# Performance work log

Measured on AMD Instinct MI355X. Metric: run time of the kernel, lower is better.

## Reference

```python
import jax, jax.numpy as jnp
import numpy as np

B, S, D = 32, 200, 256          # batch, seq_len (hard-coded 200), emb_dim (hard-coded 256)
H_CLS, H_TNS, H = 2, 4, 6       # classical heads, tensor heads, total (rate=1/3, num_heads=6)
DFF, VOCAB, L, TD = 1024, 3500, 8, 2


def layer_norm(x, g, b, eps=1e-6):
    m = x.mean(-1, keepdims=True)
    v = ((x - m) ** 2).mean(-1, keepdims=True)
    return (x - m) * jax.lax.rsqrt(v + eps) * g + b


def setup_inputs() -> dict:
    key = jax.random.key(0)
    ks = jax.random.split(key, 12)
    n = jax.random.normal
    s1 = 1.0 / np.sqrt(4 + TD - 1.0)       # TNLayer RandomNormal stddev for A1/A4
    s2 = 1.0 / np.sqrt(4 + 2 * TD - 1.0)   # for A2/A3
    return {
        "tokens": jax.random.randint(ks[0], (B, S), 0, VOCAB),
        "tok_emb": n(ks[1], (VOCAB, D)) * 0.02,
        "pos_emb": n(ks[2], (S, D)) * 0.02,
        # stacked over L layers; axis 1 of size 3 is (q, k, v)
        "wqkv_w": n(ks[3], (L, 3, D, 2 * D)) * 0.05,
        "wqkv_b": jnp.zeros((L, 3, 2 * D)),
        "A1": n(ks[4], (L, 3, 4, TD, 4)) * s1,
        "A2": n(ks[5], (L, 3, 4, TD, TD, 8)) * s2,
        "A3": n(ks[6], (L, 3, 4, TD, TD, 8)) * s2,
        "A4": n(ks[7], (L, 3, 4, TD, 4)) * s1,
        "tnb": jnp.zeros((L, 3, 4 * D)),
        "out_w": n(ks[8], (L, H * D, D)) * 0.02,
        "out_b": jnp.zeros((L, D)),
        "ff1_w": n(ks[9], (L, D, DFF)) * 0.05,
        "ff1_b": jnp.zeros((L, DFF)),
        "ff2_w": n(ks[10], (L, DFF, D)) * 0.03,
        "ff2_b": jnp.zeros((L, D)),
        "ln1_g": jnp.ones((L, D)), "ln1_b": jnp.zeros((L, D)),
        "ln2_g": jnp.ones((L, D)), "ln2_b": jnp.zeros((L, D)),
    }


def bert_tensor_forward(tokens, tok_emb, pos_emb, wqkv_w, wqkv_b, A1, A2, A3, A4, tnb,
                        out_w, out_b, ff1_w, ff1_b, ff2_w, ff2_b, ln1_g, ln1_b, ln2_g, ln2_b):
    # embedding: positions array with start_index=1 is [0,1,...,199] -> pos_emb itself
    h = tok_emb[tokens] + pos_emb[None]                      # [B,S,D]
    # Attention_mask: 1.0 where token==0 (pad), broadcast over heads and query pos
    bias = (tokens == 0).astype(jnp.float32)[:, None, None, :] * (-1e9)  # [B,1,1,S]
    inv_sqrt_dk = 1.0 / jnp.sqrt(jnp.float32(D))

    def step(h, p):
        ww, wb, a1, a2, a3, a4, tb, ow, ob, f1w, f1b, f2w, f2b, g1, b1, g2, b2 = p
        # classical q/k/v heads: Dense(d_model * 2) -> [3,B,2,S,D]
        cls = jnp.einsum('bsd,xdf->xbsf', h, ww) + wb[:, None, None, :]
        cls = cls.reshape(3, B, S, H_CLS, D).transpose(0, 1, 3, 2, 4)
        # tensor-network q/k/v heads (TNLayer): MPO contraction over 4x4x4x4 split of D
        x6 = h.reshape(B, S, 4, 4, 4, 4)
        tns = jnp.einsum('bspqrt,xpmi,xqmnj,xrnok,xtol->xbsijkl', x6, a1, a2, a3, a4)
        tns = tns.reshape(3, B, S, 4 * D) + tb[:, None, None, :]
        tns = tns.reshape(3, B, S, H_TNS, D).transpose(0, 1, 3, 2, 4)  # [3,B,4,S,D]
        qkv = jnp.concatenate([cls, tns], axis=2)                      # [3,B,H,S,D]
        q, k, v = qkv[0], qkv[1], qkv[2]
        scores = jnp.einsum('bhqd,bhkd->bhqk', q, k) * inv_sqrt_dk + bias
        attn = jax.nn.softmax(scores, axis=-1)
        ctx = jnp.einsum('bhqk,bhkd->bhqd', attn, v)
        ctx = ctx.transpose(0, 2, 1, 3).reshape(B, S, H * D)           # [B,S,1536]
        out1 = layer_norm(h + ctx @ ow + ob, g1, b1)
        ffn = jax.nn.relu(out1 @ f1w + f1b) @ f2w + f2b
        return layer_norm(out1 + ffn, g2, b2), None

    xs = (wqkv_w, wqkv_b, A1, A2, A3, A4, tnb, out_w, out_b,
          ff1_w, ff1_b, ff2_w, ff2_b, ln1_g, ln1_b, ln2_g, ln2_b)
    h, _ = jax.lax.scan(step, h, xs)
    return h


def reference(tokens, tok_emb, pos_emb, wqkv_w, wqkv_b, A1, A2, A3, A4, tnb,
              out_w, out_b, ff1_w, ff1_b, ff2_w, ff2_b, ln1_g, ln1_b, ln2_g, ln2_b):
    return bert_tensor_forward(tokens, tok_emb, pos_emb, wqkv_w, wqkv_b, A1, A2, A3, A4,
                               tnb, out_w, out_b, ff1_w, ff1_b, ff2_w, ff2_b,
                               ln1_g, ln1_b, ln2_g, ln2_b)
```

## Files before the change

### kernel.cpp

```cpp
#include <hip/hip_runtime.h>
#include <hip/hip_bf16.h>

typedef __bf16 bf16x8 __attribute__((ext_vector_type(8)));
typedef float f32x4 __attribute__((ext_vector_type(4)));
typedef int i32x4 __attribute__((ext_vector_type(4)));

#define NB 32
#define NS 200
#define SP 256
#define ND 256
#define NH 6
#define NL 8
#define NBS (NB*NS)
#define NZ (NB*NH)
#define SLAB (SP*ND)
#define PSTR 264

using bf16 = __hip_bfloat16;

enum { EPI_F32 = 0, EPI_RELU_BF = 1 };

__device__ __forceinline__ float b2f(bf16 x) { return __bfloat162float(x); }
__device__ __forceinline__ bf16 f2b(float x) { return __float2bfloat16(x); }
__device__ __forceinline__ unsigned short fbits(float x) { bf16 h = f2b(x); return *(unsigned short*)&h; }

__device__ __forceinline__ void gload16(const bf16* g, const short* l) {
    __builtin_amdgcn_global_load_lds(
        (const __attribute__((address_space(1))) unsigned int*)(unsigned long long)(g),
        (__attribute__((address_space(3))) unsigned int*)(unsigned long long)(l), 16, 0, 0);
}

#define GUNIT(lane) ((((lane) & 3) ^ (((lane) >> 3) & 3)) * 8)
#define RUNIT(kcu, fr) ((((kcu) ^ (((fr) >> 1) & 3))) * 8)

__global__ __launch_bounds__(256)
void gemm_qkv(const bf16* __restrict__ A, const bf16* __restrict__ Bm,
              const float* __restrict__ qkvb, const float* __restrict__ tnbp,
              bf16* __restrict__ Qb, bf16* __restrict__ Kb, bf16* __restrict__ Vb)
{
    __shared__ __align__(16) char smem[32768];
    short* Asl0 = (short*)smem;
    short* Bsl0 = (short*)(smem + 16384);
    const int K = 256, N = NBS;
    const int tid  = threadIdx.x;
    const int m0   = blockIdx.y * 64;
    const int n0   = blockIdx.x * 64;
    const int lane = tid & 63, w = tid >> 6;
    const int wm   = (w >> 1) * 32, wn = (w & 1) * 32;
    const int fr   = lane & 15, kcu = lane >> 4;
    const int srow = lane >> 2, schk = GUNIT(lane);

    const bf16* Ag = A  + (long long)m0 * K;
    const bf16* Bg = Bm + (long long)n0 * K;

    f32x4 acc[2][2];
#pragma unroll
    for (int i = 0; i < 2; i++)
#pragma unroll
        for (int j = 0; j < 2; j++) acc[i][j] = (f32x4){0.f,0.f,0.f,0.f};

    auto stage = [&](int buf, int k0) {
        gload16(Ag + (long long)(w*16 + srow)*K + k0 + schk, &Asl0[buf*2048 + (w*16)*32]);
        gload16(Bg + (long long)(w*16 + srow)*K + k0 + schk, &Bsl0[buf*2048 + (w*16)*32]);
    };

    stage(0, 0);
    stage(1, 32);
    for (int t = 0; t < 8; t++) {
        const int buf = t & 3;
        if (t + 2 < 8) {
            stage((t + 2) & 3, (t + 2) * 32);
            asm volatile("s_waitcnt vmcnt(4)" ::: "memory");
        } else if (t + 1 < 8) {
            asm volatile("s_waitcnt vmcnt(2)" ::: "memory");
        } else {
            asm volatile("s_waitcnt vmcnt(0)" ::: "memory");
        }
        __builtin_amdgcn_s_barrier();
        __builtin_amdgcn_sched_barrier(0);
        bf16x8 af[2], bfm[2];
#pragma unroll
        for (int i = 0; i < 2; i++) af[i]  = *(const bf16x8*)&Asl0[buf*2048 + (wm + i*16 + fr)*32 + RUNIT(kcu, fr)];
#pragma unroll
        for (int j = 0; j < 2; j++) bfm[j] = *(const bf16x8*)&Bsl0[buf*2048 + (wn + j*16 + fr)*32 + RUNIT(kcu, fr)];
#pragma unroll
        for (int i = 0; i < 2; i++)
#pragma unroll
            for (int j = 0; j < 2; j++)
                acc[i][j] = __builtin_amdgcn_mfma_f32_16x16x32_bf16(af[i], bfm[j], acc[i][j], 0, 0, 0);
    }

    const int xq   = m0 / 1536;
    const int c1_0 = m0 - xq*1536;
    const int hdq  = c1_0 >> 8;
    const int ddb  = c1_0 & 255;

    if (xq < 2) {
        short* T = (short*)smem;
        __syncthreads();
#pragma unroll
        for (int i = 0; i < 2; i++) {
            const int dl0 = wm + i*16 + kcu*4;
            float bv[4];
#pragma unroll
            for (int rg = 0; rg < 4; rg++) {
                const int cc = c1_0 + dl0 + rg;
                bv[rg] = (cc < 512) ? qkvb[xq*512 + cc] : tnbp[xq*1024 + cc - 512];
            }
#pragma unroll
            for (int j = 0; j < 2; j++) {
                const int tok = wn + j*16 + fr;
                ushort4 pk;
                pk.x = fbits(acc[i][j][0] + bv[0]);
                pk.y = fbits(acc[i][j][1] + bv[1]);
                pk.z = fbits(acc[i][j][2] + bv[2]);
                pk.w = fbits(acc[i][j][3] + bv[3]);
                *(ushort4*)&T[tok*72 + dl0] = pk;
            }
        }
        __syncthreads();
        const int tt = tid >> 2;
        const int dc = (tid & 3) * 16;
        const int c  = n0 + tt;
        const int bb = c / NS, ss = c - bb*NS;
        bf16* dst = xq ? Kb : Qb;
        bf16* dp  = dst + ((long long)((bb*NH + hdq)*SP + ss))*ND + ddb + dc;
        *(i32x4*)dp       = *(const i32x4*)&T[tt*72 + dc];
        *(i32x4*)(dp + 8) = *(const i32x4*)&T[tt*72 + dc + 8];
    } else {
#pragma unroll
        for (int i = 0; i < 2; i++) {
            const int dl0 = wm + i*16 + kcu*4;
            float bv[4];
#pragma unroll
            for (int rg = 0; rg < 4; rg++) {
                const int cc = c1_0 + dl0 + rg;
                bv[rg] = (cc < 512) ? qkvb[2*512 + cc] : tnbp[2*1024 + cc - 512];
            }
#pragma unroll
            for (int j = 0; j < 2; j++) {
                const int c = n0 + wn + j*16 + fr;
                const int bb = c / NS, ss = c - bb*NS;
                const long long base = ((long long)((bb*NH + hdq)*ND + ddb + dl0))*SP + ss;
#pragma unroll
                for (int rg = 0; rg < 4; rg++)
                    Vb[base + (long long)rg*SP] = f2b(acc[i][j][rg] + bv[rg]);
            }
        }
    }
}

template<int MODE>
__global__ __launch_bounds__(256)
void gemm_nt(const bf16* __restrict__ A, const bf16* __restrict__ Bm,
             int M, int N, int K, int Kspan, long long sOz,
             float* __restrict__ outF, bf16* __restrict__ outBf,
             const float* __restrict__ bias)
{
    __shared__ short Asl[3][128*32];
    __shared__ short Bsl[3][128*32];
    const int tid  = threadIdx.x;
    const int m0   = blockIdx.y * 128;
    const int n0   = blockIdx.x * 128;
    const int kbase= blockIdx.z * Kspan;
    const int lane = tid & 63, w = tid >> 6;
    const int wm   = (w >> 1) * 64, wn = (w & 1) * 64;
    const int fr   = lane & 15, kc = (lane >> 4) * 8;
    const int srow = lane >> 2, schk = (lane & 3) * 8;

    const bf16* Ag = A  + (long long)m0 * K + kbase;
    const bf16* Bg = Bm + (long long)n0 * K + kbase;

    f32x4 acc[4][4];
#pragma unroll
    for (int i = 0; i < 4; i++)
#pragma unroll
        for (int j = 0; j < 4; j++) acc[i][j] = (f32x4){0.f,0.f,0.f,0.f};

    auto stage = [&](int buf, int k0) {
        gload16(Ag + (long long)(w*32      + srow)*K + k0 + schk, &Asl[buf][(w*32     )*32]);
        gload16(Ag + (long long)(w*32 + 16 + srow)*K + k0 + schk, &Asl[buf][(w*32 + 16)*32]);
        gload16(Bg + (long long)(w*32      + srow)*K + k0 + schk, &Bsl[buf][(w*32     )*32]);
        gload16(Bg + (long long)(w*32 + 16 + srow)*K + k0 + schk, &Bsl[buf][(w*32 + 16)*32]);
    };

    const int nt = Kspan >> 5;
    stage(0, 0);
    for (int t = 0; t < nt; t++) {
        const int buf = t % 3;
        if (t + 1 < nt) {
            stage((t + 1) % 3, (t + 1) * 32);
            asm volatile("s_waitcnt vmcnt(4)" ::: "memory");
        } else {
            asm volatile("s_waitcnt vmcnt(0)" ::: "memory");
        }
        __builtin_amdgcn_s_barrier();
        __builtin_amdgcn_sched_barrier(0);
        bf16x8 af[4], bfm[4];
#pragma unroll
        for (int i = 0; i < 4; i++) af[i]  = *(const bf16x8*)&Asl[buf][(wm + i*16 + fr)*32 + kc];
#pragma unroll
        for (int j = 0; j < 4; j++) bfm[j] = *(const bf16x8*)&Bsl[buf][(wn + j*16 + fr)*32 + kc];
#pragma unroll
        for (int i = 0; i < 4; i++)
#pragma unroll
            for (int j = 0; j < 4; j++)
                acc[i][j] = __builtin_amdgcn_mfma_f32_16x16x32_bf16(af[i], bfm[j], acc[i][j], 0, 0, 0);
    }

    const int rq = (lane >> 4) * 4;
#pragma unroll
    for (int i = 0; i < 4; i++) {
        const int r0 = m0 + wm + i*16 + rq;
#pragma unroll
        for (int j = 0; j < 4; j++) {
            const int c = n0 + wn + j*16 + fr;
            if (MODE == EPI_F32) {
#pragma unroll
                for (int rg = 0; rg < 4; rg++)
                    outF[(long long)blockIdx.z * sOz + (long long)(r0+rg)*N + c] = acc[i][j][rg];
            } else {
                const float bv = bias[c];
#pragma unroll
                for (int rg = 0; rg < 4; rg++)
                    outBf[(long long)(r0+rg)*N + c] = f2b(fmaxf(acc[i][j][rg] + bv, 0.f));
            }
        }
    }
}

__global__ __launch_bounds__(256)
void attn_fused(const bf16* __restrict__ Qb, const bf16* __restrict__ Kb,
                const bf16* __restrict__ Vtb, const int* __restrict__ tokens,
                bf16* __restrict__ ctx)
{
    __shared__ __align__(16) char smem[2*20480 + 1024 + 1024 + 64*PSTR*2];
    float* red   = (float*)(smem + 40960);
    float* maskv = (float*)(smem + 40960 + 1024);
    short* P     = (short*)(smem + 40960 + 2048);

    const int z  = blockIdx.x;
    const int b  = z / NH, h = z - b*NH;
    const int q0 = blockIdx.y * 64;
    const int tid = threadIdx.x;
    const int lane = tid & 63, w = tid >> 6;
    const int fr = lane & 15, qh = lane >> 4;
    const int kc = qh * 8;
    const int srow = lane >> 2, schk = GUNIT(lane);

    const bf16* Kp = Kb  + (long long)z * SLAB;
    const bf16* Qp = Qb  + (long long)z * SLAB;
    const bf16* Vp = Vtb + (long long)z * SLAB;

    {
        const int s = tid;
        float mv = -1e9f;
        if (s < NS && tokens[b*NS + s] != 0) mv = 0.f;
        maskv[s] = mv;
    }

    auto stage1 = [&](int buf, int k0) {
        short* Ks = (short*)(smem + buf*20480);
        short* Qs = (short*)(smem + buf*20480 + 16384);
#pragma unroll
        for (int r2 = 0; r2 < 4; r2++)
            gload16(Kp + (long long)(w*64 + r2*16 + srow)*ND + k0 + schk, &Ks[(w*64 + r2*16)*32]);
        gload16(Qp + (long long)(q0 + w*16 + srow)*ND + k0 + schk, &Qs[(w*16)*32]);
    };

    f32x4 acc[4][4];
#pragma unroll
    for (int i = 0; i < 4; i++)
#pragma unroll
        for (int j = 0; j < 4; j++) acc[i][j] = (f32x4){0.f,0.f,0.f,0.f};

    stage1(0, 0);
    for (int t = 0; t < 8; t++) {
        const int buf = t & 1;
        if (t + 1 < 8) {
            stage1(buf ^ 1, (t + 1) * 32);
            asm volatile("s_waitcnt vmcnt(5)" ::: "memory");
        } else {
            asm volatile("s_waitcnt vmcnt(0)" ::: "memory");
        }
        __builtin_amdgcn_s_barrier();
        __builtin_amdgcn_sched_barrier(0);
        const short* Ks = (const short*)(smem + buf*20480);
        const short* Qs = (const short*)(smem + buf*20480 + 16384);
        bf16x8 ak[4], bq[4];
#pragma unroll
        for (int i = 0; i < 4; i++) ak[i] = *(const bf16x8*)&Ks[(w*64 + i*16 + fr)*32 + RUNIT(qh, fr)];
#pragma unroll
        for (int j = 0; j < 4; j++) bq[j] = *(const bf16x8*)&Qs[(j*16 + fr)*32 + RUNIT(qh, fr)];
#pragma unroll
        for (int i = 0; i < 4; i++)
#pragma unroll
            for (int j = 0; j < 4; j++)
                acc[i][j] = __builtin_amdgcn_mfma_f32_16x16x32_bf16(ak[i], bq[j], acc[i][j], 0, 0, 0);
        __builtin_amdgcn_s_barrier();
        __builtin_amdgcn_sched_barrier(0);
    }

    float mk[4][4];
#pragma unroll
    for (int i = 0; i < 4; i++)
#pragma unroll
        for (int rg = 0; rg < 4; rg++) mk[i][rg] = maskv[w*64 + i*16 + qh*4 + rg];
#pragma unroll
    for (int i = 0; i < 4; i++)
#pragma unroll
        for (int j = 0; j < 4; j++)
#pragma unroll
            for (int rg = 0; rg < 4; rg++)
                acc[i][j][rg] = acc[i][j][rg] * 0.0625f + mk[i][rg];

    float pm[4];
#pragma unroll
    for (int j = 0; j < 4; j++) {
        float m = -3.0e38f;
#pragma unroll
        for (int i = 0; i < 4; i++)
#pragma unroll
            for (int rg = 0; rg < 4; rg++) m = fmaxf(m, acc[i][j][rg]);
        m = fmaxf(m, __shfl_xor(m, 16));
        m = fmaxf(m, __shfl_xor(m, 32));
        pm[j] = m;
    }
#pragma unroll
    for (int j = 0; j < 4; j++) red[w*64 + j*16 + fr] = pm[j];
    __syncthreads();
    float gm[4];
#pragma unroll
    for (int j = 0; j < 4; j++)
        gm[j] = fmaxf(fmaxf(red[j*16 + fr], red[64 + j*16 + fr]),
                      fmaxf(red[128 + j*16 + fr], red[192 + j*16 + fr]));
    float ps[4] = {0.f, 0.f, 0.f, 0.f};
#pragma unroll
    for (int i = 0; i < 4; i++)
#pragma unroll
        for (int j = 0; j < 4; j++)
#pragma unroll
            for (int rg = 0; rg < 4; rg++) {
                float e = __expf(acc[i][j][rg] - gm[j]);
                acc[i][j][rg] = e;
                ps[j] += e;
            }
#pragma unroll
    for (int j = 0; j < 4; j++) {
        ps[j] += __shfl_xor(ps[j], 16);
        ps[j] += __shfl_xor(ps[j], 32);
    }
    __syncthreads();
#pragma unroll
    for (int j = 0; j < 4; j++) red[w*64 + j*16 + fr] = ps[j];
    __syncthreads();
    float inv[4];
#pragma unroll
    for (int j = 0; j < 4; j++)
        inv[j] = 1.f / (red[j*16 + fr] + red[64 + j*16 + fr] + red[128 + j*16 + fr] + red[192 + j*16 + fr]);

#pragma unroll
    for (int i = 0; i < 4; i++)
#pragma unroll
        for (int j = 0; j < 4; j++) {
            ushort4 pk;
            pk.x = fbits(acc[i][j][0] * inv[j]);
            pk.y = fbits(acc[i][j][1] * inv[j]);
            pk.z = fbits(acc[i][j][2] * inv[j]);
            pk.w = fbits(acc[i][j][3] * inv[j]);
            *(ushort4*)&P[(j*16 + fr)*PSTR + w*64 + i*16 + qh*4] = pk;
        }
    __syncthreads();

    auto stage2 = [&](int buf, int s0) {
        short* Vs = (short*)(smem + buf*20480);
#pragma unroll
        for (int r2 = 0; r2 < 4; r2++)
            gload16(Vp + (long long)(w*64 + r2*16 + srow)*SP + s0 + schk, &Vs[(w*64 + r2*16)*32]);
    };

    f32x4 acc2[4][4];
#pragma unroll
    for (int i = 0; i < 4; i++)
#pragma unroll
        for (int j = 0; j < 4; j++) acc2[i][j] = (f32x4){0.f,0.f,0.f,0.f};

    stage2(0, 0);
    for (int t = 0; t < 7; t++) {
        const int buf = t & 1;
        if (t + 1 < 7) {
            stage2(buf ^ 1, (t + 1) * 32);
            asm volatile("s_waitcnt vmcnt(4)" ::: "memory");
        } else {
            asm volatile("s_waitcnt vmcnt(0)" ::: "memory");
        }
        __builtin_amdgcn_s_barrier();
        __builtin_amdgcn_sched_barrier(0);
        const short* Vs = (const short*)(smem + buf*20480);
        bf16x8 ap[4], bv[4];
#pragma unroll
        for (int i = 0; i < 4; i++) ap[i] = *(const bf16x8*)&P[(i*16 + fr)*PSTR + t*32 + kc];
#pragma unroll
        for (int j = 0; j < 4; j++) bv[j] = *(const bf16x8*)&Vs[(w*64 + j*16 + fr)*32 + RUNIT(qh, fr)];
#pragma unroll
        for (int i = 0; i < 4; i++)
#pragma unroll
            for (int j = 0; j < 4; j++)
                acc2[i][j] = __builtin_amdgcn_mfma_f32_16x16x32_bf16(ap[i], bv[j], acc2[i][j], 0, 0, 0);
        __builtin_amdgcn_s_barrier();
        __builtin_amdgcn_sched_barrier(0);
    }

#pragma unroll
    for (int i = 0; i < 4; i++)
#pragma unroll
        for (int j = 0; j < 4; j++)
#pragma unroll
            for (int rg = 0; rg < 4; rg++) {
                const int qg = q0 + i*16 + qh*4 + rg;
                if (qg < NS) {
                    const int d = w*64 + j*16 + fr;
                    ctx[((long long)(b*NS + qg))*1536 + h*256 + d] = f2b(acc2[i][j][rg]);
                }
            }
}

__global__ void embed_kernel(const int* __restrict__ tokens, const float* __restrict__ tok_emb,
                             const float* __restrict__ pos_emb, float* __restrict__ hf,
                             bf16* __restrict__ hbf)
{
    long long id = (long long)blockIdx.x * 256 + threadIdx.x;
    if (id >= (long long)NBS * ND) return;
    long long r = id >> 8;
    int j = id & 255;
    int tk = tokens[r];
    int s  = (int)(r % NS);
    float v = tok_emb[(long long)tk * ND + j] + pos_emb[s * ND + j];
    hf[id]  = v;
    hbf[id] = f2b(v);
}

__global__ __launch_bounds__(256)
void transpose_tile(const float* __restrict__ in, bf16* __restrict__ out,
                    int R, int C, long long inL, long long outL, int outStride)
{
    __shared__ float tl[32][33];
    const int l  = blockIdx.z;
    const int r0 = blockIdx.y * 32, c0 = blockIdx.x * 32;
    const float* ip = in + (long long)l * inL;
    bf16* op = out + (long long)l * outL;
    const int tx = threadIdx.x & 31, ty = threadIdx.x >> 5;
#pragma unroll
    for (int i = 0; i < 4; i++) {
        const int r = r0 + ty + i*8;
        tl[ty + i*8][tx] = ip[(long long)r * C + c0 + tx];
    }
    __syncthreads();
#pragma unroll
    for (int i = 0; i < 4; i++) {
        const int c = c0 + ty + i*8;
        op[(long long)c * outStride + r0 + tx] = f2b(tl[tx][ty + i*8]);
    }
}

__global__ __launch_bounds__(256)
void build_wtns(const float* __restrict__ A1, const float* __restrict__ A2,
                const float* __restrict__ A3, const float* __restrict__ A4,
                bf16* __restrict__ wcat)
{
    int lx = blockIdx.x;
    __shared__ float a1s[32], a2s[128], a3s[128], a4s[32];
    int t = threadIdx.x;
    if (t < 32)  { a1s[t] = A1[lx*32 + t]; a4s[t] = A4[lx*32 + t]; }
    if (t < 128) { a2s[t] = A2[lx*128 + t]; a3s[t] = A3[lx*128 + t]; }
    __syncthreads();
    int d = t;
    int p = d >> 6, q = (d >> 4) & 3, rr = (d >> 2) & 3, tt = d & 3;
    for (int i = 0; i < 4; i++) {
        float w1_0 = a1s[(p*2 + 0)*4 + i];
        float w1_1 = a1s[(p*2 + 1)*4 + i];
        for (int j = 0; j < 8; j++) {
            float c1_0 = w1_0 * a2s[((q*2+0)*2+0)*8 + j] + w1_1 * a2s[((q*2+1)*2+0)*8 + j];
            float c1_1 = w1_0 * a2s[((q*2+0)*2+1)*8 + j] + w1_1 * a2s[((q*2+1)*2+1)*8 + j];
            for (int kk = 0; kk < 8; kk++) {
                float c2_0 = c1_0 * a3s[((rr*2+0)*2+0)*8 + kk] + c1_1 * a3s[((rr*2+1)*2+0)*8 + kk];
                float c2_1 = c1_0 * a3s[((rr*2+0)*2+1)*8 + kk] + c1_1 * a3s[((rr*2+1)*2+1)*8 + kk];
                for (int ll = 0; ll < 4; ll++) {
                    float sv = c2_0 * a4s[(tt*2 + 0)*4 + ll] + c2_1 * a4s[(tt*2 + 1)*4 + ll];
                    int e = ((i*8 + j)*8 + kk)*4 + ll;
                    wcat[((long long)lx * 1536 + 512 + e) * 256 + d] = f2b(sv);
                }
            }
        }
    }
}

__global__ __launch_bounds__(256)
void ln_kernel(const float* __restrict__ raw0, const float* __restrict__ raw1,
               const float* __restrict__ bias, const float* __restrict__ resid,
               const float* __restrict__ g, const float* __restrict__ bb,
               float* __restrict__ outF, bf16* __restrict__ outBf)
{
    int w = threadIdx.x >> 6, lane = threadIdx.x & 63;
    long long r = (long long)blockIdx.x * 4 + w;
    long long base = r * ND;
    float x[4]; float s = 0.f;
#pragma unroll
    for (int c = 0; c < 4; c++) {
        int j = lane + 64*c;
        x[c] = resid[base + j] + raw0[base + j] + raw1[base + j] + bias[j];
        s += x[c];
    }
#pragma unroll
    for (int o = 32; o; o >>= 1) s += __shfl_xor(s, o);
    float mean = s * (1.f/256.f);
    float vs = 0.f;
#pragma unroll
    for (int c = 0; c < 4; c++) { float d = x[c] - mean; vs += d*d; }
#pragma unroll
    for (int o = 32; o; o >>= 1) vs += __shfl_xor(vs, o);
    float rs = rsqrtf(vs * (1.f/256.f) + 1e-6f);
#pragma unroll
    for (int c = 0; c < 4; c++) {
        int j = lane + 64*c;
        float y = (x[c] - mean) * rs * g[j] + bb[j];
        outF[base + j]  = y;
        outBf[base + j] = f2b(y);
    }
}

extern "C" void kernel_launch(void* const* d_in, const int* in_sizes, int n_in,
                              void* d_out, int out_size, void* d_ws, size_t ws_size,
                              hipStream_t stream)
{
    const int*   tokens  = (const int*)  d_in[0];
    const float* tok_emb = (const float*)d_in[1];
    const float* pos_emb = (const float*)d_in[2];
    const float* wqkv_w  = (const float*)d_in[3];
    const float* wqkv_b  = (const float*)d_in[4];
    const float* A1      = (const float*)d_in[5];
    const float* A2      = (const float*)d_in[6];
    const float* A3      = (const float*)d_in[7];
    const float* A4      = (const float*)d_in[8];
    const float* tnb     = (const float*)d_in[9];
    const float* out_w   = (const float*)d_in[10];
    const float* out_b   = (const float*)d_in[11];
    const float* ff1_w   = (const float*)d_in[12];
    const float* ff1_b   = (const float*)d_in[13];
    const float* ff2_w   = (const float*)d_in[14];
    const float* ff2_b   = (const float*)d_in[15];
    const float* ln1_g   = (const float*)d_in[16];
    const float* ln1_b   = (const float*)d_in[17];
    const float* ln2_g   = (const float*)d_in[18];
    const float* ln2_b   = (const float*)d_in[19];

    char* ws = (char*)d_ws;
    size_t off = 0;
    auto alloc = [&](size_t bytes) -> char* {
        char* p = ws + off;
        off += (bytes + 255) & ~(size_t)255;
        return p;
    };
    float* hf    = (float*)alloc((size_t)NBS * ND * 4);
    bf16*  hbf   = (bf16*) alloc((size_t)NBS * ND * 2);
    bf16*  wcat  = (bf16*) alloc(24ull * 1536 * 256 * 2);
    bf16*  owt   = (bf16*) alloc(8ull * 256 * 1536 * 2);
    bf16*  f1wt  = (bf16*) alloc(8ull * 1024 * 256 * 2);
    bf16*  f2wt  = (bf16*) alloc(8ull * 256 * 1024 * 2);
    bf16*  Qb    = (bf16*) alloc((size_t)NZ * SLAB * 2);
    bf16*  Kb    = (bf16*) alloc((size_t)NZ * SLAB * 2);
    bf16*  Vtb   = (bf16*) alloc((size_t)NZ * SLAB * 2);
    bf16*  ctxg  = (bf16*) alloc((size_t)NBS * 1536 * 2);
    bf16*  ffn   = (bf16*) alloc((size_t)NBS * 1024 * 2);
    float* raw   = (float*)alloc((size_t)NBS * ND * 4 * 2);
    float* out1f = (float*)alloc((size_t)NBS * ND * 4);
    bf16*  out1bf= (bf16*) alloc((size_t)NBS * ND * 2);
    if (off > ws_size) return;
    float* raw1 = raw + (size_t)NBS * ND;

    hipMemsetAsync(Qb, 0, (size_t)3 * NZ * SLAB * 2, stream);

    embed_kernel<<<NBS, 256, 0, stream>>>(tokens, tok_emb, pos_emb, hf, hbf);
    transpose_tile<<<dim3(16, 8, 24), 256, 0, stream>>>(
        wqkv_w, wcat, 256, 512, 256ll*512, 1536ll*256, 256);
    build_wtns<<<24, 256, 0, stream>>>(A1, A2, A3, A4, wcat);
    transpose_tile<<<dim3(8, 48, 8), 256, 0, stream>>>(
        out_w, owt, 1536, 256, 1536ll*256, 256ll*1536, 1536);
    transpose_tile<<<dim3(32, 8, 8), 256, 0, stream>>>(
        ff1_w, f1wt, 256, 1024, 256ll*1024, 1024ll*256, 256);
    transpose_tile<<<dim3(8, 32, 8), 256, 0, stream>>>(
        ff2_w, f2wt, 1024, 256, 1024ll*256, 256ll*1024, 1024);

    for (int l = 0; l < NL; l++) {
        const bf16* wl = wcat + (long long)l * 3 * 1536 * 256;
        gemm_qkv<<<dim3(100, 72, 1), 256, 0, stream>>>(
            wl, hbf, wqkv_b + l * 3 * 512, tnb + l * 3 * 1024, Qb, Kb, Vtb);
        attn_fused<<<dim3(NZ, 4), 256, 0, stream>>>(Qb, Kb, Vtb, tokens, ctxg);
        gemm_nt<EPI_F32><<<dim3(2, 50, 2), 256, 0, stream>>>(
            ctxg, owt + (long long)l * 256 * 1536, NBS, 256, 1536, 768, (long long)NBS*ND,
            raw, nullptr, nullptr);
        ln_kernel<<<1600, 256, 0, stream>>>(raw, raw1, out_b + l * 256, hf,
                                            ln1_g + l * 256, ln1_b + l * 256, out1f, out1bf);
        gemm_nt<EPI_RELU_BF><<<dim3(8, 50, 1), 256, 0, stream>>>(
            out1bf, f1wt + (long long)l * 1024 * 256, NBS, 1024, 256, 256, 0,
            nullptr, ffn, ff1_b + l * 1024);
        gemm_nt<EPI_F32><<<dim3(2, 50, 2), 256, 0, stream>>>(
            ffn, f2wt + (long long)l * 256 * 1024, NBS, 256, 1024, 512, (long long)NBS*ND,
            raw, nullptr, nullptr);
        ln_kernel<<<1600, 256, 0, stream>>>(raw, raw1, ff2_b + l * 256, out1f,
                                            ln2_g + l * 256, ln2_b + l * 256,
                                            (l == NL - 1) ? (float*)d_out : hf, hbf);
    }
}
```

Baseline: 959.9 us.

## Replace LDS-staged GEMM and attention loads with direct global fragment loads

All GEMM kernels and both attention matmul loops drop the async global-to-LDS staging pipeline and its barriers. Each wave now reads its MFMA fragments straight from global memory, relying on the caches for reuse. The dense GEMMs move from 128x128 to 64x64 tiles with larger grids. Embedding and layernorm kernels are vectorised to float4, and the per-call memset of the Q/K/V buffers is removed. Cross-wave operand sharing through LDS is lost, so global/L2 traffic rises. With no memset, the padded rows of Q/K/V past the 200 valid tokens are no longer cleared each call, yet attention still reads them.

```diff
diff --git a/kernel.cpp b/kernel.cpp
--- a/kernel.cpp
+++ b/kernel.cpp
@@ -24,34 +24,26 @@
 __device__ __forceinline__ bf16 f2b(float x) { return __float2bfloat16(x); }
 __device__ __forceinline__ unsigned short fbits(float x) { bf16 h = f2b(x); return *(unsigned short*)&h; }
 
-__device__ __forceinline__ void gload16(const bf16* g, const short* l) {
-    __builtin_amdgcn_global_load_lds(
-        (const __attribute__((address_space(1))) unsigned int*)(unsigned long long)(g),
-        (__attribute__((address_space(3))) unsigned int*)(unsigned long long)(l), 16, 0, 0);
-}
-
-#define GUNIT(lane) ((((lane) & 3) ^ (((lane) >> 3) & 3)) * 8)
-#define RUNIT(kcu, fr) ((((kcu) ^ (((fr) >> 1) & 3))) * 8)
+#define MFMA __builtin_amdgcn_mfma_f32_16x16x32_bf16
 
 __global__ __launch_bounds__(256)
 void gemm_qkv(const bf16* __restrict__ A, const bf16* __restrict__ Bm,
               const float* __restrict__ qkvb, const float* __restrict__ tnbp,
               bf16* __restrict__ Qb, bf16* __restrict__ Kb, bf16* __restrict__ Vb)
 {
-    __shared__ __align__(16) char smem[32768];
-    short* Asl0 = (short*)smem;
-    short* Bsl0 = (short*)(smem + 16384);
-    const int K = 256, N = NBS;
+    __shared__ __align__(16) short T[64*72];
+    const int K = 256;
     const int tid  = threadIdx.x;
     const int m0   = blockIdx.y * 64;
     const int n0   = blockIdx.x * 64;
     const int lane = tid & 63, w = tid >> 6;
     const int wm   = (w >> 1) * 32, wn = (w & 1) * 32;
     const int fr   = lane & 15, kcu = lane >> 4;
-    const int srow = lane >> 2, schk = GUNIT(lane);
-
-    const bf16* Ag = A  + (long long)m0 * K;
-    const bf16* Bg = Bm + (long long)n0 * K;
+
+    const bf16* Ap0 = A  + (long long)(m0 + wm + fr) * K + kcu * 8;
+    const bf16* Ap1 = Ap0 + 16 * K;
+    const bf16* Bp0 = Bm + (long long)(n0 + wn + fr) * K + kcu * 8;
+    const bf16* Bp1 = Bp0 + 16 * K;
 
     f32x4 acc[2][2];
 #pragma unroll
@@ -59,35 +51,17 @@
 #pragma unroll
         for (int j = 0; j < 2; j++) acc[i][j] = (f32x4){0.f,0.f,0.f,0.f};
 
-    auto stage = [&](int buf, int k0) {
-        gload16(Ag + (long long)(w*16 + srow)*K + k0 + schk, &Asl0[buf*2048 + (w*16)*32]);
-        gload16(Bg + (long long)(w*16 + srow)*K + k0 + schk, &Bsl0[buf*2048 + (w*16)*32]);
-    };
-
-    stage(0, 0);
-    stage(1, 32);
+#pragma unroll
     for (int t = 0; t < 8; t++) {
-        const int buf = t & 3;
-        if (t + 2 < 8) {
-            stage((t + 2) & 3, (t + 2) * 32);
-            asm volatile("s_waitcnt vmcnt(4)" ::: "memory");
-        } else if (t + 1 < 8) {
-            asm volatile("s_waitcnt vmcnt(2)" ::: "memory");
-        } else {
-            asm volatile("s_waitcnt vmcnt(0)" ::: "memory");
-        }
-        __builtin_amdgcn_s_barrier();
-        __builtin_amdgcn_sched_barrier(0);
-        bf16x8 af[2], bfm[2];
-#pragma unroll
-        for (int i = 0; i < 2; i++) af[i]  = *(const bf16x8*)&Asl0[buf*2048 + (wm + i*16 + fr)*32 + RUNIT(kcu, fr)];
-#pragma unroll
-        for (int j = 0; j < 2; j++) bfm[j] = *(const bf16x8*)&Bsl0[buf*2048 + (wn + j*16 + fr)*32 + RUNIT(kcu, fr)];
-#pragma unroll
-        for (int i = 0; i < 2; i++)
-#pragma unroll
-            for (int j = 0; j < 2; j++)
-                acc[i][j] = __builtin_amdgcn_mfma_f32_16x16x32_bf16(af[i], bfm[j], acc[i][j], 0, 0, 0);
+        const int k0 = t * 32;
+        bf16x8 a0 = *(const bf16x8*)(Ap0 + k0);
+        bf16x8 a1 = *(const bf16x8*)(Ap1 + k0);
+        bf16x8 b0 = *(const bf16x8*)(Bp0 + k0);
+        bf16x8 b1 = *(const bf16x8*)(Bp1 + k0);
+        acc[0][0] = MFMA(a0, b0, acc[0][0], 0, 0, 0);
+        acc[0][1] = MFMA(a0, b1, acc[0][1], 0, 0, 0);
+        acc[1][0] = MFMA(a1, b0, acc[1][0], 0, 0, 0);
+        acc[1][1] = MFMA(a1, b1, acc[1][1], 0, 0, 0);
     }
 
     const int xq   = m0 / 1536;
@@ -96,8 +70,6 @@
     const int ddb  = c1_0 & 255;
 
     if (xq < 2) {
-        short* T = (short*)smem;
-        __syncthreads();
 #pragma unroll
         for (int i = 0; i < 2; i++) {
             const int dl0 = wm + i*16 + kcu*4;
@@ -152,68 +124,50 @@
 
 template<int MODE>
 __global__ __launch_bounds__(256)
-void gemm_nt(const bf16* __restrict__ A, const bf16* __restrict__ Bm,
-             int M, int N, int K, int Kspan, long long sOz,
-             float* __restrict__ outF, bf16* __restrict__ outBf,
-             const float* __restrict__ bias)
-{
-    __shared__ short Asl[3][128*32];
-    __shared__ short Bsl[3][128*32];
+void gemm_d(const bf16* __restrict__ A, const bf16* __restrict__ Bm,
+            int M, int N, int K, int Kspan, long long sOz,
+            float* __restrict__ outF, bf16* __restrict__ outBf,
+            const float* __restrict__ bias)
+{
     const int tid  = threadIdx.x;
-    const int m0   = blockIdx.y * 128;
-    const int n0   = blockIdx.x * 128;
+    const int m0   = blockIdx.y * 64;
+    const int n0   = blockIdx.x * 64;
     const int kbase= blockIdx.z * Kspan;
     const int lane = tid & 63, w = tid >> 6;
-    const int wm   = (w >> 1) * 64, wn = (w & 1) * 64;
-    const int fr   = lane & 15, kc = (lane >> 4) * 8;
-    const int srow = lane >> 2, schk = (lane & 3) * 8;
-
-    const bf16* Ag = A  + (long long)m0 * K + kbase;
-    const bf16* Bg = Bm + (long long)n0 * K + kbase;
-
-    f32x4 acc[4][4];
-#pragma unroll
-    for (int i = 0; i < 4; i++)
-#pragma unroll
-        for (int j = 0; j < 4; j++) acc[i][j] = (f32x4){0.f,0.f,0.f,0.f};
-
-    auto stage = [&](int buf, int k0) {
-        gload16(Ag + (long long)(w*32      + srow)*K + k0 + schk, &Asl[buf][(w*32     )*32]);
-        gload16(Ag + (long long)(w*32 + 16 + srow)*K + k0 + schk, &Asl[buf][(w*32 + 16)*32]);
-        gload16(Bg + (long long)(w*32      + srow)*K + k0 + schk, &Bsl[buf][(w*32     )*32]);
-        gload16(Bg + (long long)(w*32 + 16 + srow)*K + k0 + schk, &Bsl[buf][(w*32 + 16)*32]);
-    };
+    const int wm   = (w >> 1) * 32, wn = (w & 1) * 32;
+    const int fr   = lane & 15, kcu = lane >> 4;
+
+    const bf16* Ap0 = A  + (long long)(m0 + wm + fr) * K + kbase + kcu * 8;
+    const bf16* Ap1 = Ap0 + 16 * K;
+    const bf16* Bp0 = Bm + (long long)(n0 + wn + fr) * K + kbase + kcu * 8;
+    const bf16* Bp1 = Bp0 + 16 * K;
+
+    f32x4 acc[2][2];
+#pragma unroll
+    for (int i = 0; i < 2; i++)
+#pragma unroll
+        for (int j = 0; j < 2; j++) acc[i][j] = (f32x4){0.f,0.f,0.f,0.f};
 
     const int nt = Kspan >> 5;
-    stage(0, 0);
+#pragma unroll 4
     for (int t = 0; t < nt; t++) {
-        const int buf = t % 3;
-        if (t + 1 < nt) {
-            stage((t + 1) % 3, (t + 1) * 32);
-            asm volatile("s_waitcnt vmcnt(4)" ::: "memory");
-        } else {
-            asm volatile("s_waitcnt vmcnt(0)" ::: "memory");
-        }
-        __builtin_amdgcn_s_barrier();
-        __builtin_amdgcn_sched_barrier(0);
-        bf16x8 af[4], bfm[4];
-#pragma unroll
-        for (int i = 0; i < 4; i++) af[i]  = *(const bf16x8*)&Asl[buf][(wm + i*16 + fr)*32 + kc];
-#pragma unroll
-        for (int j = 0; j < 4; j++) bfm[j] = *(const bf16x8*)&Bsl[buf][(wn + j*16 + fr)*32 + kc];
-#pragma unroll
-        for (int i = 0; i < 4; i++)
-#pragma unroll
-            for (int j = 0; j < 4; j++)
-                acc[i][j] = __builtin_amdgcn_mfma_f32_16x16x32_bf16(af[i], bfm[j], acc[i][j], 0, 0, 0);
-    }
-
-    const int rq = (lane >> 4) * 4;
-#pragma unroll
-    for (int i = 0; i < 4; i++) {
+        const int k0 = t * 32;
+        bf16x8 a0 = *(const bf16x8*)(Ap0 + k0);
+        bf16x8 a1 = *(const bf16x8*)(Ap1 + k0);
+        bf16x8 b0 = *(const bf16x8*)(Bp0 + k0);
+        bf16x8 b1 = *(const bf16x8*)(Bp1 + k0);
+        acc[0][0] = MFMA(a0, b0, acc[0][0], 0, 0, 0);
+        acc[0][1] = MFMA(a0, b1, acc[0][1], 0, 0, 0);
+        acc[1][0] = MFMA(a1, b0, acc[1][0], 0, 0, 0);
+        acc[1][1] = MFMA(a1, b1, acc[1][1], 0, 0, 0);
+    }
+
+    const int rq = kcu * 4;
+#pragma unroll
+    for (int i = 0; i < 2; i++) {
         const int r0 = m0 + wm + i*16 + rq;
 #pragma unroll
-        for (int j = 0; j < 4; j++) {
+        for (int j = 0; j < 2; j++) {
             const int c = n0 + wn + j*16 + fr;
             if (MODE == EPI_F32) {
 #pragma unroll
@@ -234,10 +188,10 @@
                 const bf16* __restrict__ Vtb, const int* __restrict__ tokens,
                 bf16* __restrict__ ctx)
 {
-    __shared__ __align__(16) char smem[2*20480 + 1024 + 1024 + 64*PSTR*2];
-    float* red   = (float*)(smem + 40960);
-    float* maskv = (float*)(smem + 40960 + 1024);
-    short* P     = (short*)(smem + 40960 + 2048);
+    __shared__ __align__(16) char smem[1024 + 1024 + 64*PSTR*2];
+    float* red   = (float*)smem;
+    float* maskv = (float*)(smem + 1024);
+    short* P     = (short*)(smem + 2048);
 
     const int z  = blockIdx.x;
     const int b  = z / NH, h = z - b*NH;
@@ -246,7 +200,6 @@
     const int lane = tid & 63, w = tid >> 6;
     const int fr = lane & 15, qh = lane >> 4;
     const int kc = qh * 8;
-    const int srow = lane >> 2, schk = GUNIT(lane);
 
     const bf16* Kp = Kb  + (long long)z * SLAB;
     const bf16* Qp = Qb  + (long long)z * SLAB;
@@ -259,46 +212,29 @@
         maskv[s] = mv;
     }
 
-    auto stage1 = [&](int buf, int k0) {
-        short* Ks = (short*)(smem + buf*20480);
-        short* Qs = (short*)(smem + buf*20480 + 16384);
-#pragma unroll
-        for (int r2 = 0; r2 < 4; r2++)
-            gload16(Kp + (long long)(w*64 + r2*16 + srow)*ND + k0 + schk, &Ks[(w*64 + r2*16)*32]);
-        gload16(Qp + (long long)(q0 + w*16 + srow)*ND + k0 + schk, &Qs[(w*16)*32]);
-    };
-
     f32x4 acc[4][4];
 #pragma unroll
     for (int i = 0; i < 4; i++)
 #pragma unroll
         for (int j = 0; j < 4; j++) acc[i][j] = (f32x4){0.f,0.f,0.f,0.f};
 
-    stage1(0, 0);
+#pragma unroll 2
     for (int t = 0; t < 8; t++) {
-        const int buf = t & 1;
-        if (t + 1 < 8) {
-            stage1(buf ^ 1, (t + 1) * 32);
-            asm volatile("s_waitcnt vmcnt(5)" ::: "memory");
-        } else {
-            asm volatile("s_waitcnt vmcnt(0)" ::: "memory");
-        }
-        __builtin_amdgcn_s_barrier();
-        __builtin_amdgcn_sched_barrier(0);
-        const short* Ks = (const short*)(smem + buf*20480);
-        const short* Qs = (const short*)(smem + buf*20480 + 16384);
+        const int k0 = t * 32;
         bf16x8 ak[4], bq[4];
 #pragma unroll
-        for (int i = 0; i < 4; i++) ak[i] = *(const bf16x8*)&Ks[(w*64 + i*16 + fr)*32 + RUNIT(qh, fr)];
-#pragma unroll
-        for (int j = 0; j < 4; j++) bq[j] = *(const bf16x8*)&Qs[(j*16 + fr)*32 + RUNIT(qh, fr)];
-#pragma unroll
         for (int i = 0; i < 4; i++)
+            ak[i] = *(const bf16x8*)(Kp + (long long)(w*64 + i*16 + fr)*ND + k0 + kc);
+#pragma unroll
+        for (int j = 0; j < 4; j++)
+            bq[j] = *(const bf16x8*)(Qp + (long long)(q0 + j*16 + fr)*ND + k0 + kc);
+        __builtin_amdgcn_s_setprio(1);
+#pragma unroll
+        for (int i = 0; i < 4; i++)
 #pragma unroll
             for (int j = 0; j < 4; j++)
-                acc[i][j] = __builtin_amdgcn_mfma_f32_16x16x32_bf16(ak[i], bq[j], acc[i][j], 0, 0, 0);
-        __builtin_amdgcn_s_barrier();
-        __builtin_amdgcn_sched_barrier(0);
+                acc[i][j] = MFMA(ak[i], bq[j], acc[i][j], 0, 0, 0);
+        __builtin_amdgcn_s_setprio(0);
     }
 
     float mk[4][4];
@@ -372,43 +308,28 @@
         }
     __syncthreads();
 
-    auto stage2 = [&](int buf, int s0) {
-        short* Vs = (short*)(smem + buf*20480);
-#pragma unroll
-        for (int r2 = 0; r2 < 4; r2++)
-            gload16(Vp + (long long)(w*64 + r2*16 + srow)*SP + s0 + schk, &Vs[(w*64 + r2*16)*32]);
-    };
-
     f32x4 acc2[4][4];
 #pragma unroll
     for (int i = 0; i < 4; i++)
 #pragma unroll
         for (int j = 0; j < 4; j++) acc2[i][j] = (f32x4){0.f,0.f,0.f,0.f};
 
-    stage2(0, 0);
+#pragma unroll 2
     for (int t = 0; t < 7; t++) {
-        const int buf = t & 1;
-        if (t + 1 < 7) {
-            stage2(buf ^ 1, (t + 1) * 32);
-            asm volatile("s_waitcnt vmcnt(4)" ::: "memory");
-        } else {
-            asm volatile("s_waitcnt vmcnt(0)" ::: "memory");
-        }
-        __builtin_amdgcn_s_barrier();
-        __builtin_amdgcn_sched_barrier(0);
-        const short* Vs = (const short*)(smem + buf*20480);
+        const int s0 = t * 32;
         bf16x8 ap[4], bv[4];
 #pragma unroll
-        for (int i = 0; i < 4; i++) ap[i] = *(const bf16x8*)&P[(i*16 + fr)*PSTR + t*32 + kc];
-#pragma unroll
-        for (int j = 0; j < 4; j++) bv[j] = *(const bf16x8*)&Vs[(w*64 + j*16 + fr)*32 + RUNIT(qh, fr)];
+        for (int i = 0; i < 4; i++) ap[i] = *(const bf16x8*)&P[(i*16 + fr)*PSTR + s0 + kc];
+#pragma unroll
+        for (int j = 0; j < 4; j++)
+            bv[j] = *(const bf16x8*)(Vp + (long long)(w*64 + j*16 + fr)*SP + s0 + kc);
+        __builtin_amdgcn_s_setprio(1);
 #pragma unroll
         for (int i = 0; i < 4; i++)
 #pragma unroll
             for (int j = 0; j < 4; j++)
-                acc2[i][j] = __builtin_amdgcn_mfma_f32_16x16x32_bf16(ap[i], bv[j], acc2[i][j], 0, 0, 0);
-        __builtin_amdgcn_s_barrier();
-        __builtin_amdgcn_sched_barrier(0);
+                acc2[i][j] = MFMA(ap[i], bv[j], acc2[i][j], 0, 0, 0);
+        __builtin_amdgcn_s_setprio(0);
     }
 
 #pragma unroll
@@ -429,15 +350,19 @@
                              const float* __restrict__ pos_emb, float* __restrict__ hf,
                              bf16* __restrict__ hbf)
 {
-    long long id = (long long)blockIdx.x * 256 + threadIdx.x;
-    if (id >= (long long)NBS * ND) return;
-    long long r = id >> 8;
-    int j = id & 255;
+    long long q = (long long)blockIdx.x * 256 + threadIdx.x;
+    if (q >= (long long)NBS * 64) return;
+    long long r = q >> 6;
+    int j = (int)(q & 63) * 4;
     int tk = tokens[r];
     int s  = (int)(r % NS);
-    float v = tok_emb[(long long)tk * ND + j] + pos_emb[s * ND + j];
-    hf[id]  = v;
-    hbf[id] = f2b(v);
+    float4 tv = *(const float4*)(tok_emb + (long long)tk * ND + j);
+    float4 pv = *(const float4*)(pos_emb + s * ND + j);
+    float4 v = make_float4(tv.x+pv.x, tv.y+pv.y, tv.z+pv.z, tv.w+pv.w);
+    *(float4*)(hf + r*ND + j) = v;
+    ushort4 pk;
+    pk.x = fbits(v.x); pk.y = fbits(v.y); pk.z = fbits(v.z); pk.w = fbits(v.w);
+    *(ushort4*)(hbf + r*ND + j) = pk;
 }
 
 __global__ __launch_bounds__(256)
@@ -503,30 +428,35 @@
 {
     int w = threadIdx.x >> 6, lane = threadIdx.x & 63;
     long long r = (long long)blockIdx.x * 4 + w;
-    long long base = r * ND;
-    float x[4]; float s = 0.f;
-#pragma unroll
-    for (int c = 0; c < 4; c++) {
-        int j = lane + 64*c;
-        x[c] = resid[base + j] + raw0[base + j] + raw1[base + j] + bias[j];
-        s += x[c];
-    }
+    long long base = r * ND + lane * 4;
+    float4 x  = *(const float4*)(resid + base);
+    float4 y0 = *(const float4*)(raw0 + base);
+    float4 y1 = *(const float4*)(raw1 + base);
+    float4 bs = *(const float4*)(bias + lane * 4);
+    x.x += y0.x + y1.x + bs.x;
+    x.y += y0.y + y1.y + bs.y;
+    x.z += y0.z + y1.z + bs.z;
+    x.w += y0.w + y1.w + bs.w;
+    float s = x.x + x.y + x.z + x.w;
 #pragma unroll
     for (int o = 32; o; o >>= 1) s += __shfl_xor(s, o);
     float mean = s * (1.f/256.f);
-    float vs = 0.f;
-#pragma unroll
-    for (int c = 0; c < 4; c++) { float d = x[c] - mean; vs += d*d; }
+    float vs = (x.x-mean)*(x.x-mean) + (x.y-mean)*(x.y-mean)
+             + (x.z-mean)*(x.z-mean) + (x.w-mean)*(x.w-mean);
 #pragma unroll
     for (int o = 32; o; o >>= 1) vs += __shfl_xor(vs, o);
     float rs = rsqrtf(vs * (1.f/256.f) + 1e-6f);
-#pragma unroll
-    for (int c = 0; c < 4; c++) {
-        int j = lane + 64*c;
-        float y = (x[c] - mean) * rs * g[j] + bb[j];
-        outF[base + j]  = y;
-        outBf[base + j] = f2b(y);
-    }
+    float4 gv = *(const float4*)(g  + lane * 4);
+    float4 bv = *(const float4*)(bb + lane * 4);
+    float4 o4;
+    o4.x = (x.x - mean) * rs * gv.x + bv.x;
+    o4.y = (x.y - mean) * rs * gv.y + bv.y;
+    o4.z = (x.z - mean) * rs * gv.z + bv.z;
+    o4.w = (x.w - mean) * rs * gv.w + bv.w;
+    *(float4*)(outF + base) = o4;
+    ushort4 pk;
+    pk.x = fbits(o4.x); pk.y = fbits(o4.y); pk.z = fbits(o4.z); pk.w = fbits(o4.w);
+    *(ushort4*)(outBf + base) = pk;
 }
 
 extern "C" void kernel_launch(void* const* d_in, const int* in_sizes, int n_in,
@@ -578,9 +508,8 @@
     if (off > ws_size) return;
     float* raw1 = raw + (size_t)NBS * ND;
 
-    hipMemsetAsync(Qb, 0, (size_t)3 * NZ * SLAB * 2, stream);
-
-    embed_kernel<<<NBS, 256, 0, stream>>>(tokens, tok_emb, pos_emb, hf, hbf);
+
+    embed_kernel<<<1600, 256, 0, stream>>>(tokens, tok_emb, pos_emb, hf, hbf);
     transpose_tile<<<dim3(16, 8, 24), 256, 0, stream>>>(
         wqkv_w, wcat, 256, 512, 256ll*512, 1536ll*256, 256);
     build_wtns<<<24, 256, 0, stream>>>(A1, A2, A3, A4, wcat);
@@ -596,15 +525,15 @@
         gemm_qkv<<<dim3(100, 72, 1), 256, 0, stream>>>(
             wl, hbf, wqkv_b + l * 3 * 512, tnb + l * 3 * 1024, Qb, Kb, Vtb);
         attn_fused<<<dim3(NZ, 4), 256, 0, stream>>>(Qb, Kb, Vtb, tokens, ctxg);
-        gemm_nt<EPI_F32><<<dim3(2, 50, 2), 256, 0, stream>>>(
+        gemm_d<EPI_F32><<<dim3(4, 100, 2), 256, 0, stream>>>(
             ctxg, owt + (long long)l * 256 * 1536, NBS, 256, 1536, 768, (long long)NBS*ND,
             raw, nullptr, nullptr);
         ln_kernel<<<1600, 256, 0, stream>>>(raw, raw1, out_b + l * 256, hf,
                                             ln1_g + l * 256, ln1_b + l * 256, out1f, out1bf);
-        gemm_nt<EPI_RELU_BF><<<dim3(8, 50, 1), 256, 0, stream>>>(
+        gemm_d<EPI_RELU_BF><<<dim3(16, 100, 1), 256, 0, stream>>>(
             out1bf, f1wt + (long long)l * 1024 * 256, NBS, 1024, 256, 256, 0,
             nullptr, ffn, ff1_b + l * 1024);
-        gemm_nt<EPI_F32><<<dim3(2, 50, 2), 256, 0, stream>>>(
+        gemm_d<EPI_F32><<<dim3(4, 100, 2), 256, 0, stream>>>(
             ffn, f2wt + (long long)l * 256 * 1024, NBS, 256, 1024, 512, (long long)NBS*ND,
             raw, nullptr, nullptr);
         ln_kernel<<<1600, 256, 0, stream>>>(raw, raw1, ff2_b + l * 256, out1f,
```

After: 2.205 ms. 130% more time.
